# Performance work log

Hardware: AMD Instinct MI355X
Metric: run time of the kernel (lower is better)

Reference implementation:

```python
import jax, jax.numpy as jnp
import numpy as np

H = 16  # n_heads

def setup_inputs() -> dict:
    key = jax.random.key(0)
    k1, k2, k3, k4 = jax.random.split(key, 4)
    B, S, D = 2, 2048, 1024
    query = jax.random.normal(k1, (B, S, D), dtype=jnp.float32)
    pos_emb = jax.random.normal(k2, (S, D), dtype=jnp.float32)
    w_qkv = jax.random.normal(k3, (D, 3 * D), dtype=jnp.float32) * (D ** -0.5)
    w_out = jax.random.normal(k4, (D, D), dtype=jnp.float32) * (D ** -0.5)
    return {"query": query, "pos_emb": pos_emb, "w_qkv": w_qkv, "w_out": w_out}

def reference(query, pos_emb, w_qkv, w_out):
    B, S, D = query.shape
    d_k = D // H
    # ape=True: pos_fn applied to input before QKV projection (additive APE)
    x = query + pos_emb[None, :, :]
    # fused QKV projection; torch view(B,S,H,3*d_k) + chunk(3,-1) == reshape(B,S,H,3,d_k)
    qkv = jnp.einsum('bsd,de->bse', x, w_qkv).reshape(B, S, H, 3, d_k)
    qkv = jnp.transpose(qkv, (0, 2, 1, 3, 4))  # [B,H,S,3,d_k]
    q, k, v = qkv[..., 0, :], qkv[..., 1, :], qkv[..., 2, :]
    scale = d_k ** -0.5
    scores = jnp.einsum('bhqd,bhkd->bhqk', q, k) * scale  # [B,H,S,S]
    attn = jax.nn.softmax(scores, axis=-1)  # dropout is identity in eval
    o = jnp.einsum('bhqk,bhkd->bhqd', attn, v)
    o = jnp.transpose(o, (0, 2, 1, 3)).reshape(B, S, D)
    return jnp.einsum('bsd,de->bse', o, w_out)
```

## Files before the change

### kernel.cpp

```cpp
#include <hip/hip_runtime.h>

#define SS 2048
#define DD 1024
#define N3 3072

typedef unsigned short u16;
typedef unsigned int u32;
typedef __attribute__((ext_vector_type(8))) short bf16x8;
typedef __attribute__((ext_vector_type(4))) short bf16x4;
typedef __attribute__((ext_vector_type(4))) float f32x4;

__device__ __forceinline__ u16 f2bf(float f) {
    u32 u = __float_as_uint(f);
    u32 r = u + 0x7fffu + ((u >> 16) & 1u);
    return (u16)(r >> 16);
}

__device__ __forceinline__ float fast_exp2(float x) {
    return __builtin_amdgcn_exp2f(x);
}

__device__ __forceinline__ void async_cp16(u16* lds, const u16* g) {
    __builtin_amdgcn_global_load_lds((const __attribute__((address_space(1))) u32*)g,
                                     (__attribute__((address_space(3))) u32*)lds, 16, 0, 0);
}

__device__ __forceinline__ f32x4 mfma16(bf16x4 a, bf16x4 b, f32x4 c) {
    return __builtin_amdgcn_mfma_f32_16x16x16bf16_1k(a, b, c, 0, 0, 0);
}

__global__ __launch_bounds__(256)
void prep_all(const float* __restrict__ q, const float* __restrict__ pos,
              const float* __restrict__ wqkv, const float* __restrict__ wout,
              u16* __restrict__ x, u16* __restrict__ wqkvT, u16* __restrict__ woutT)
{
    __shared__ float t[32][33];
    const int bx = blockIdx.x;

    if (bx < 4096) {
        const size_t i = ((size_t)bx * 256 + threadIdx.x) * 4;
        float4 a = *(const float4*)(q + i);
        float4 p = *(const float4*)(pos + (i & (size_t)(SS * DD - 1)));
        uint2 r;
        r.x = (u32)f2bf(a.x + p.x) | ((u32)f2bf(a.y + p.y) << 16);
        r.y = (u32)f2bf(a.z + p.z) | ((u32)f2bf(a.w + p.w) << 16);
        *(uint2*)(x + i) = r;
        return;
    }

    const int isq = bx < 7168;
    const int tt  = isq ? (bx - 4096) : (bx - 7168);
    const int nx  = isq ? 96 : 32;
    const int N   = isq ? N3 : DD;
    const float* W = isq ? wqkv : wout;
    u16* WT = isq ? wqkvT : woutT;

    const int x0 = (tt % nx) * 32, y0 = (tt / nx) * 32;
    const int tx = threadIdx.x & 31, ty = threadIdx.x >> 5;
#pragma unroll
    for (int i = 0; i < 4; ++i)
        t[ty + i * 8][tx] = W[(size_t)(y0 + ty + i * 8) * N + x0 + tx];
    __syncthreads();
#pragma unroll
    for (int i = 0; i < 4; ++i) {
        const int n = x0 + ty + i * 8;
        float v = t[tx][ty + i * 8];
        if (isq && (n % 192) < 64) v *= 0.18033688f;
        WT[(size_t)n * DD + y0 + tx] = f2bf(v);
    }
}

__global__ __launch_bounds__(256)
void transpose_v(const u16* __restrict__ qkv, u16* __restrict__ vt)
{
    __shared__ u16 t[64][72];
    const int bx = blockIdx.x;
    const int bh = bx >> 5, st = bx & 31;
    const int b = bh >> 4, h = bh & 15;
    const int r = threadIdx.x >> 2, c16 = (threadIdx.x & 3) * 16;

    const u16* src = qkv + (size_t)(b * SS + st * 64 + r) * N3 + h * 192 + 128 + c16;
    *(uint4*)&t[r][c16]     = *(const uint4*)src;
    *(uint4*)&t[r][c16 + 8] = *(const uint4*)(src + 8);
    __syncthreads();

    union { uint4 q[2]; u16 hh[16]; } u;
#pragma unroll
    for (int j = 0; j < 16; ++j) u.hh[j] = t[c16 + j][r];
    uint4* dst = (uint4*)(vt + ((size_t)bh * 64 + r) * SS + st * 64 + c16);
    dst[0] = u.q[0]; dst[1] = u.q[1];
}

template <int OUT_BF16, int NT>
__global__ __launch_bounds__(256)
void gemm_mfma(const u16* __restrict__ A, const u16* __restrict__ BT,
               void* __restrict__ Cv, int M, int N, int K)
{
    constexpr int FR = NT / 32;
    __shared__ u16 As[128 * 64];
    __shared__ u16 Bs[NT * 64];

    const int tid = threadIdx.x;
    const int lane = tid & 63, wv = tid >> 6;
    const int quad = lane >> 4, l16 = lane & 15;
    const int m0 = blockIdx.y * 128, n0 = blockIdx.x * NT;

    const int arow = wv * 32 + (lane >> 3);
    const int pc   = lane & 7;
    const int lcA  = pc ^ (arow & 7);
    const u16* agp = A + (size_t)(m0 + arow) * K + lcA * 8;
    u16* alp = As + arow * 64 + pc * 8;

    const int brow = (NT == 128) ? (wv * 32 + (lane >> 3)) : (wv * 8 + (lane >> 3));
    const int lcB  = pc ^ (brow & 7);
    const u16* bgp = BT + (size_t)(n0 + brow) * K + lcB * 8;
    u16* blp = Bs + brow * 64 + pc * 8;

    const int moff = (wv >> 1) * 64, noff = (wv & 1) * (NT / 2);

    f32x4 acc[4][FR];
#pragma unroll
    for (int i = 0; i < 4; ++i)
#pragma unroll
        for (int j = 0; j < FR; ++j) acc[i][j] = {0.f, 0.f, 0.f, 0.f};

    const int swf = l16 & 7;

    for (int k0 = 0; k0 < K; k0 += 64) {
#pragma unroll
        for (int s = 0; s < 4; ++s)
            async_cp16(alp + s * 8 * 64, agp + (size_t)(s * 8) * K + k0);
        if constexpr (NT == 128) {
#pragma unroll
            for (int s = 0; s < 4; ++s)
                async_cp16(blp + s * 8 * 64, bgp + (size_t)(s * 8) * K + k0);
        } else {
#pragma unroll
            for (int s = 0; s < 2; ++s)
                async_cp16(blp + s * 32 * 64, bgp + (size_t)(s * 32) * K + k0);
        }
        __syncthreads();

#pragma unroll
        for (int ks = 0; ks < 2; ++ks) {
            bf16x8 af[4], bfr[FR];
#pragma unroll
            for (int t = 0; t < 4; ++t)
                af[t] = *(const bf16x8*)&As[(moff + t * 16 + l16) * 64 + (((ks * 4 + quad) ^ swf) << 3)];
#pragma unroll
            for (int t = 0; t < FR; ++t)
                bfr[t] = *(const bf16x8*)&Bs[(noff + t * 16 + l16) * 64 + (((ks * 4 + quad) ^ swf) << 3)];
#pragma unroll
            for (int mt = 0; mt < 4; ++mt)
#pragma unroll
                for (int nt = 0; nt < FR; ++nt)
                    acc[mt][nt] = __builtin_amdgcn_mfma_f32_16x16x32_bf16(af[mt], bfr[nt], acc[mt][nt], 0, 0, 0);
        }
        __syncthreads();
    }

#pragma unroll
    for (int mt = 0; mt < 4; ++mt)
#pragma unroll
        for (int r = 0; r < 4; ++r) {
            const size_t row = m0 + moff + mt * 16 + quad * 4 + r;
            if (OUT_BF16) {
                u16* cp = (u16*)Cv + row * N + n0 + noff + l16;
#pragma unroll
                for (int nt = 0; nt < FR; ++nt) cp[nt * 16] = f2bf(acc[mt][nt][r]);
            } else {
                float* cp = (float*)Cv + row * N + n0 + noff + l16;
#pragma unroll
                for (int nt = 0; nt < FR; ++nt) cp[nt * 16] = acc[mt][nt][r];
            }
        }
}

__global__ __launch_bounds__(512, 4)
void attn_mfma(const u16* __restrict__ qkv, const u16* __restrict__ vt, u16* __restrict__ o)
{
    __shared__ __align__(16) u16 smem[32768];

    const int tid = threadIdx.x;
    const int lane = tid & 63, wv = tid >> 6;
    const int grp = wv >> 2, w4 = wv & 3;
    const int quad = lane >> 4, l16 = lane & 15;
    const int bx = blockIdx.x;
    const int bh = bx & 31, qt = bx >> 5;
    const int h = bh & 15, b = bh >> 4;

    const size_t hb = (size_t)b * SS * N3 + h * 192;
    const int q0 = qt * 128 + w4 * 32;
    const int sw = l16 & 7;

    bf16x8 qf[2][2];
#pragma unroll
    for (int mt = 0; mt < 2; ++mt)
#pragma unroll
        for (int ks = 0; ks < 2; ++ks)
            qf[mt][ks] = *(const bf16x8*)(qkv + hb + (size_t)(q0 + mt * 16 + l16) * N3 + ks * 32 + quad * 8);

    f32x4 po[2][4];
#pragma unroll
    for (int mt = 0; mt < 2; ++mt)
#pragma unroll
        for (int nt = 0; nt < 4; ++nt) po[mt][nt] = {0.f, 0.f, 0.f, 0.f};
    float lrun[2] = {0.f, 0.f};

    const int lrow = lane >> 3, pc8 = lane & 7, lc = pc8 ^ lrow;
    const int srow = w4 * 16;
    const int kt0 = grp * 16;

    const u16* kgp = qkv + hb + 64 + (size_t)(kt0 * 64 + srow + lrow) * N3 + lc * 8;
    const u16* vgp = vt + ((size_t)bh * 64 + srow + lrow) * SS + kt0 * 64 + lc * 8;

    u16* const ksA = smem + (grp * 2) * 4096 + (srow + lrow) * 64 + pc8 * 8;
    u16* const ksB = ksA + 4096;
    u16* const vsA = smem + 16384 + (grp * 2) * 4096 + (srow + lrow) * 64 + pc8 * 8;
    u16* const vsB = vsA + 4096;

    async_cp16(ksA,       kgp);
    async_cp16(ksA + 512, kgp + (size_t)8 * N3);
    async_cp16(vsA,       vgp);
    async_cp16(vsA + 512, vgp + (size_t)8 * SS);

    for (int it = 0; it < 16; ++it) {
        const int p = it & 1;
        asm volatile("s_waitcnt vmcnt(0) lgkmcnt(0)\n\ts_barrier" ::: "memory");
        if (it < 15) {
            const size_t ko = (size_t)(it + 1) * 64;
            u16* kb = p ? ksA : ksB;
            u16* vb = p ? vsA : vsB;
            async_cp16(kb,       kgp + ko * N3);
            async_cp16(kb + 512, kgp + ko * N3 + (size_t)8 * N3);
            async_cp16(vb,       vgp + ko);
            async_cp16(vb + 512, vgp + ko + (size_t)8 * SS);
        }
        const u16* kbuf = smem + (grp * 2 + p) * 4096;
        const u16* vbuf = smem + 16384 + (grp * 2 + p) * 4096;

        f32x4 sf[2][4];
#pragma unroll
        for (int mt = 0; mt < 2; ++mt)
#pragma unroll
            for (int kn = 0; kn < 4; ++kn) sf[mt][kn] = {0.f, 0.f, 0.f, 0.f};
        __builtin_amdgcn_s_setprio(1);
#pragma unroll
        for (int ks = 0; ks < 2; ++ks)
#pragma unroll
            for (int kn = 0; kn < 4; ++kn) {
                bf16x8 kf = *(const bf16x8*)&kbuf[(kn * 16 + l16) * 64 + (((ks * 4 + quad) ^ sw) << 3)];
#pragma unroll
                for (int mt = 0; mt < 2; ++mt)
                    sf[mt][kn] = __builtin_amdgcn_mfma_f32_16x16x32_bf16(kf, qf[mt][ks], sf[mt][kn], 0, 0, 0);
            }
        __builtin_amdgcn_s_setprio(0);

        u32 SW[2][4][2];
#pragma unroll
        for (int mt = 0; mt < 2; ++mt) {
            float ls = 0.f;
#pragma unroll
            for (int kn = 0; kn < 4; ++kn) {
                const float p0 = fast_exp2(sf[mt][kn][0]);
                const float p1 = fast_exp2(sf[mt][kn][1]);
                const float p2 = fast_exp2(sf[mt][kn][2]);
                const float p3 = fast_exp2(sf[mt][kn][3]);
                ls += (p0 + p1) + (p2 + p3);
                SW[mt][kn][0] = __builtin_amdgcn_perm(__float_as_uint(p1), __float_as_uint(p0), 0x07060302u);
                SW[mt][kn][1] = __builtin_amdgcn_perm(__float_as_uint(p3), __float_as_uint(p2), 0x07060302u);
            }
            lrun[mt] += ls;
        }

        __builtin_amdgcn_s_setprio(1);
#pragma unroll
        for (int kn = 0; kn < 4; ++kn) {
            bf16x4 vf[4];
#pragma unroll
            for (int nt = 0; nt < 4; ++nt)
                vf[nt] = *(const bf16x4*)&vbuf[(nt * 16 + l16) * 64 + (((2 * kn + (quad >> 1)) ^ sw) << 3) + ((quad & 1) << 2)];
#pragma unroll
            for (int mt = 0; mt < 2; ++mt) {
                union { bf16x4 v; u32 w[2]; } pu;
                pu.w[0] = SW[mt][kn][0];
                pu.w[1] = SW[mt][kn][1];
#pragma unroll
                for (int nt = 0; nt < 4; ++nt)
                    po[mt][nt] = mfma16(vf[nt], pu.v, po[mt][nt]);
            }
        }
        __builtin_amdgcn_s_setprio(0);
    }

    __syncthreads();

#pragma unroll
    for (int mt = 0; mt < 2; ++mt) {
        lrun[mt] += __shfl_xor(lrun[mt], 16, 64);
        lrun[mt] += __shfl_xor(lrun[mt], 32, 64);
    }

    float* xch = (float*)smem;
    if (grp == 1) {
        float* d = xch + (w4 * 64 + lane) * 36;
#pragma unroll
        for (int mt = 0; mt < 2; ++mt)
#pragma unroll
            for (int nt = 0; nt < 4; ++nt)
                *(f32x4*)(d + mt * 16 + nt * 4) = po[mt][nt];
        d[32] = lrun[0]; d[33] = lrun[1];
    }
    __syncthreads();
    if (grp == 0) {
        const float* s = xch + (w4 * 64 + lane) * 36;
#pragma unroll
        for (int mt = 0; mt < 2; ++mt)
#pragma unroll
            for (int nt = 0; nt < 4; ++nt)
                po[mt][nt] = po[mt][nt] + *(const f32x4*)(s + mt * 16 + nt * 4);
        lrun[0] += s[32]; lrun[1] += s[33];

#pragma unroll
        for (int mt = 0; mt < 2; ++mt) {
            const float linv = 1.f / lrun[mt];
            const size_t row = (size_t)b * SS + q0 + mt * 16 + l16;
#pragma unroll
            for (int nt = 0; nt < 4; ++nt) {
                const u32 h0 = (u32)f2bf(po[mt][nt][0] * linv) | ((u32)f2bf(po[mt][nt][1] * linv) << 16);
                const u32 h1 = (u32)f2bf(po[mt][nt][2] * linv) | ((u32)f2bf(po[mt][nt][3] * linv) << 16);
                uint2 wp; wp.x = h0; wp.y = h1;
                *(uint2*)(o + row * DD + h * 64 + nt * 16 + quad * 4) = wp;
            }
        }
    }
}

extern "C" void kernel_launch(void* const* d_in, const int* in_sizes, int n_in,
                              void* d_out, int out_size, void* d_ws, size_t ws_size,
                              hipStream_t stream)
{
    const float* query  = (const float*)d_in[0];
    const float* posemb = (const float*)d_in[1];
    const float* w_qkv  = (const float*)d_in[2];
    const float* w_out  = (const float*)d_in[3];
    float* out = (float*)d_out;

    u16* xb    = (u16*)d_ws;
    u16* wqkvT = xb    + (size_t)4096 * 1024;
    u16* woutT = wqkvT + (size_t)3072 * 1024;
    u16* qkv   = woutT + (size_t)1024 * 1024;
    u16* ob    = qkv   + (size_t)4096 * 3072;
    u16* vtb   = ob    + (size_t)4096 * 1024;

    prep_all<<<8192, 256, 0, stream>>>(query, posemb, w_qkv, w_out, xb, wqkvT, woutT);

    gemm_mfma<1, 128><<<dim3(N3 / 128, 4096 / 128), 256, 0, stream>>>(xb, wqkvT, (void*)qkv, 4096, N3, DD);

    transpose_v<<<1024, 256, 0, stream>>>(qkv, vtb);

    attn_mfma<<<dim3(512, 1, 1), 512, 0, stream>>>(qkv, vtb, ob);

    gemm_mfma<0, 64><<<dim3(DD / 64, 4096 / 128), 256, 0, stream>>>(ob, woutT, (void*)out, 4096, DD, DD);
}
```

Measured before the change: 188.8 us.

## Add 256x256-tile double-buffered MFMA GEMM for QKV projection

Replaces the 128x128 QKV projection GEMM with a new 256x256 tile kernel using 512 threads, 128KB of dynamic LDS, async global-to-LDS copies with double buffering, and XOR-swizzled LDS layout. Larger tiles raise arithmetic intensity and cut global traffic per FLOP, and the double buffer overlaps loads with MFMA work. The trade-off is fewer blocks (192), which is below the CU count, plus heavy register and LDS use, so occupancy drops.

Result: no change. 185.2 us (-1.9%).

```diff
diff --git a/kernel.cpp b/kernel.cpp
--- a/kernel.cpp
+++ b/kernel.cpp
@@ -89,6 +89,79 @@
     for (int j = 0; j < 16; ++j) u.hh[j] = t[c16 + j][r];
     uint4* dst = (uint4*)(vt + ((size_t)bh * 64 + r) * SS + st * 64 + c16);
     dst[0] = u.q[0]; dst[1] = u.q[1];
+}
+
+__global__ __launch_bounds__(512, 2)
+void gemm256(const u16* __restrict__ A, const u16* __restrict__ BT,
+             u16* __restrict__ C, int M, int N, int K)
+{
+    extern __shared__ __align__(16) u16 smem[];
+
+    const int tid = threadIdx.x;
+    const int lane = tid & 63;
+    const int wv = tid >> 6;
+    const int quad = lane >> 4, l16 = lane & 15;
+    const int wm = wv >> 2, wn = wv & 3;
+    const int m0 = blockIdx.y * 256, n0 = blockIdx.x * 256;
+    const int sw = l16 & 7;
+
+    const int srow = tid >> 3, pc = tid & 7, lc = pc ^ (srow & 7);
+    const u16* agp = A  + (size_t)(m0 + srow) * K + lc * 8;
+    const u16* bgp = BT + (size_t)(n0 + srow) * K + lc * 8;
+    u16* const asw = smem +         srow * 64 + pc * 8;
+    u16* const bsw = smem + 32768 + srow * 64 + pc * 8;
+
+    auto stage = [&](int buf, int k0) {
+#pragma unroll
+        for (int s = 0; s < 4; ++s)
+            async_cp16(asw + buf * 16384 + s * 4096, agp + (size_t)(s * 64) * K + k0);
+#pragma unroll
+        for (int s = 0; s < 4; ++s)
+            async_cp16(bsw + buf * 16384 + s * 4096, bgp + (size_t)(s * 64) * K + k0);
+    };
+
+    f32x4 acc[8][4];
+#pragma unroll
+    for (int i = 0; i < 8; ++i)
+#pragma unroll
+        for (int j = 0; j < 4; ++j) acc[i][j] = {0.f, 0.f, 0.f, 0.f};
+
+    stage(0, 0);
+
+    const int NT = K / 64;
+    for (int t = 0; t < NT; ++t) {
+        const int p = t & 1;
+        asm volatile("s_waitcnt vmcnt(0) lgkmcnt(0)\n\ts_barrier" ::: "memory");
+        if (t + 1 < NT) stage(p ^ 1, (t + 1) * 64);
+
+        const u16* Ab = smem +         p * 16384;
+        const u16* Bb = smem + 32768 + p * 16384;
+
+#pragma unroll
+        for (int ks = 0; ks < 2; ++ks) {
+            bf16x8 bfr[4];
+#pragma unroll
+            for (int nt = 0; nt < 4; ++nt)
+                bfr[nt] = *(const bf16x8*)&Bb[(wn * 64 + nt * 16 + l16) * 64 + (((ks * 4 + quad) ^ sw) << 3)];
+#pragma unroll
+            for (int mt = 0; mt < 8; ++mt) {
+                bf16x8 af = *(const bf16x8*)&Ab[(wm * 128 + mt * 16 + l16) * 64 + (((ks * 4 + quad) ^ sw) << 3)];
+#pragma unroll
+                for (int nt = 0; nt < 4; ++nt)
+                    acc[mt][nt] = __builtin_amdgcn_mfma_f32_16x16x32_bf16(af, bfr[nt], acc[mt][nt], 0, 0, 0);
+            }
+        }
+    }
+
+#pragma unroll
+    for (int mt = 0; mt < 8; ++mt)
+#pragma unroll
+        for (int r = 0; r < 4; ++r) {
+            const size_t row = m0 + wm * 128 + mt * 16 + quad * 4 + r;
+            u16* cp = C + row * N + n0 + wn * 64 + l16;
+#pragma unroll
+            for (int nt = 0; nt < 4; ++nt) cp[nt * 16] = f2bf(acc[mt][nt][r]);
+        }
 }
 
 template <int OUT_BF16, int NT>
@@ -353,9 +426,16 @@
     u16* ob    = qkv   + (size_t)4096 * 3072;
     u16* vtb   = ob    + (size_t)4096 * 1024;
 
+    static bool lds_init = false;
+    if (!lds_init) {
+        hipFuncSetAttribute((const void*)gemm256,
+                            hipFuncAttributeMaxDynamicSharedMemorySize, 131072);
+        lds_init = true;
+    }
+
     prep_all<<<8192, 256, 0, stream>>>(query, posemb, w_qkv, w_out, xb, wqkvT, woutT);
 
-    gemm_mfma<1, 128><<<dim3(N3 / 128, 4096 / 128), 256, 0, stream>>>(xb, wqkvT, (void*)qkv, 4096, N3, DD);
+    gemm256<<<dim3(N3 / 256, 4096 / 256), 512, 131072, stream>>>(xb, wqkvT, qkv, 4096, N3, DD);
 
     transpose_v<<<1024, 256, 0, stream>>>(qkv, vtb);
 
```
